# Performance work log

Measured on AMD Instinct MI355X. Metric: run time of the kernel, lower is better.

Reference implementation:

```python
import jax, jax.numpy as jnp
import numpy as np

LMAX = 6
NUM_COEFFS = (LMAX + 1) ** 2  # 49
REPEATS = np.array([2 * l + 1 for l in range(LMAX + 1)])  # coefficients per degree


def so3_linear(x, w, b):
    """Block-diagonal per-degree linear: x [N, 49, Cin], w [lmax+1, Cin, Cout], b [Cout].
    Bias is added only to the degree-0 (scalar) coefficient."""
    w_exp = jnp.repeat(w, REPEATS, axis=0)  # [49, Cin, Cout]
    out = jnp.einsum('nic,ico->nio', x, w_exp)
    return out.at[:, 0, :].add(b)


def setup_inputs() -> dict:
    key = jax.random.key(0)
    ks = jax.random.split(key, 10)
    N, C, H = 1024, 128, 256
    res = 18
    s = 0.05
    return {
        'node_feats': jax.random.normal(ks[0], (N, NUM_COEFFS, C), jnp.float32),
        'w1': jax.random.normal(ks[1], (LMAX + 1, C, H), jnp.float32) * s,
        'b1': jnp.zeros((H,), jnp.float32),
        'w2': jax.random.normal(ks[2], (LMAX + 1, H, C), jnp.float32) * s,
        'b2': jnp.zeros((C,), jnp.float32),
        'ws': jax.random.normal(ks[3], (C, H), jnp.float32) * s,
        'bs': jnp.zeros((H,), jnp.float32),
        'g1': jax.random.normal(ks[4], (H, H), jnp.float32) * s,
        'g2': jax.random.normal(ks[5], (H, H), jnp.float32) * s,
        'g3': jax.random.normal(ks[6], (H, H), jnp.float32) * s,
        'to_grid_mat': jax.random.normal(ks[7], (res, res, NUM_COEFFS), jnp.float32) * s,
        'from_grid_mat': jax.random.normal(ks[8], (res, res, NUM_COEFFS), jnp.float32) * s,
    }


def reference(node_feats, w1, b1, w2, b2, ws, bs, g1, g2, g3, to_grid_mat, from_grid_mat):
    # separable-S2 scalar gating branch: MLP on the l=0 coefficient  [N,1,H]
    gating = jax.nn.silu(jnp.einsum('nic,ch->nih', node_feats[:, 0:1], ws) + bs)
    # SO3 linear 1  [N,49,H]
    x = so3_linear(node_feats, w1, b1)
    # spherical harmonics -> grid  [N, beta, alpha, H]
    grid = jnp.einsum('bai,nih->nbah', to_grid_mat, x)
    # grid MLP (bias-free) with SiLU between layers
    grid = jax.nn.silu(jnp.einsum('nbah,hk->nbak', grid, g1))
    grid = jax.nn.silu(jnp.einsum('nbak,km->nbam', grid, g2))
    grid = jnp.einsum('nbam,mh->nbah', grid, g3)
    # grid -> spherical harmonics  [N,49,H]
    x = jnp.einsum('bai,nbah->nih', from_grid_mat, grid)
    # separable S2: replace l=0 component with gated scalars
    x = jnp.concatenate((gating, x[:, 1:]), axis=1)
    # SO3 linear 2  [N,49,C_out]
    return so3_linear(x, w2, b2)
```

## Files before the change

kernel.cpp:

```cpp
#include <hip/hip_runtime.h>
#include <hip/hip_bf16.h>

typedef __attribute__((ext_vector_type(8))) short bf16x8;
typedef __attribute__((ext_vector_type(4))) float f32x4;

#define MFMA(a,b,c) __builtin_amdgcn_mfma_f32_16x16x32_bf16((a),(b),(c),0,0,0)

#define WS_W1T 0
#define WS_W2T 229376
#define WS_G1T 458752
#define WS_TGP 655360
#define WS_FGT 679936
#define WS_TOTAL 704512

__device__ __forceinline__ ushort f2b(float f) {
  __hip_bfloat16 h = __float2bfloat16(f);
  ushort u; __builtin_memcpy(&u, &h, 2); return u;
}
__device__ __forceinline__ float silu_f(float x) { return x / (1.f + __expf(-x)); }
__device__ __forceinline__ bf16x8 ld8(const ushort* p) {
  return *reinterpret_cast<const bf16x8*>(p);
}

__global__ void prep_kernel(const float* __restrict__ w1, const float* __restrict__ w2,
                            const float* __restrict__ g1, const float* __restrict__ g2,
                            const float* __restrict__ g3, const float* __restrict__ tg,
                            const float* __restrict__ fg, ushort* __restrict__ o) {
  int idx = blockIdx.x * blockDim.x + threadIdx.x;
  if (idx >= WS_TOTAL) return;
  float v;
  if (idx < WS_W2T) {
    int l = idx >> 15, rem = idx & 32767, h = rem >> 7, c = rem & 127;
    v = w1[(l << 15) + c * 256 + h];
  } else if (idx < WS_G1T) {
    int j = idx - WS_W2T;
    int l = j >> 15, rem = j & 32767, oo = rem >> 8, h = rem & 255;
    v = w2[(l << 15) + h * 128 + oo];
  } else if (idx < WS_TGP) {
    int j = idx - WS_G1T;
    int m = j >> 16, r = j & 65535, n2 = r >> 8, k = r & 255;
    const float* g = (m == 0) ? g1 : ((m == 1) ? g2 : g3);
    v = g[k * 256 + n2];
  } else if (idx < WS_FGT) {
    int j = idx - WS_TGP, r = j >> 6, i2 = j & 63;
    v = (r < 324 && i2 < 49) ? tg[r * 49 + i2] : 0.f;
  } else {
    int j = idx - WS_FGT, i2 = j / 384, r = j % 384;
    v = (i2 < 49 && r < 324) ? fg[r * 49 + i2] : 0.f;
  }
  o[idx] = f2b(v);
}

__global__ __launch_bounds__(512, 1) void ffn_main(
    const float* __restrict__ nf, const float* __restrict__ b1,
    const float* __restrict__ b2, const float* __restrict__ wsg,
    const float* __restrict__ bs, const ushort* __restrict__ wbf,
    float* __restrict__ out)
{
  __shared__ __align__(16) ushort sm[35840];
  ushort* s_G   = sm;
  ushort* s_xbT = sm + 16896;
  float*  s_gat = reinterpret_cast<float*>(sm + 35328);
  ushort* s_GT  = s_xbT;
  ushort* s_nf  = s_G;
  ushort* s_xo  = s_G;

  const int tid  = threadIdx.x;
  const int lane = tid & 63;
  const int wv   = tid >> 6;
  const int lr   = lane & 15;
  const int lk   = lane >> 4;

  const float* nfp = nf + (size_t)blockIdx.x * 6272;

  {
    uint4 z = {0,0,0,0};
    for (int idx = tid; idx < 2304; idx += 512)
      *reinterpret_cast<uint4*>(&s_xbT[idx * 8]) = z;
    for (int idx = tid; idx < 52 * 32; idx += 512) {
      int r = idx >> 5, c4 = (idx & 31) << 2;
      float4 v = (r < 49) ? *reinterpret_cast<const float4*>(nfp + (r << 7) + c4)
                          : make_float4(0.f, 0.f, 0.f, 0.f);
      ushort4 pk = make_ushort4(f2b(v.x), f2b(v.y), f2b(v.z), f2b(v.w));
      *reinterpret_cast<ushort4*>(&s_nf[r * 136 + c4]) = pk;
    }
    if (tid < 256) {
      float a = bs[tid];
      #pragma unroll 4
      for (int c = 0; c < 128; ++c) a = fmaf(nfp[c], wsg[(c << 8) + tid], a);
      s_gat[tid] = silu_f(a);
    }
  }
  __syncthreads();

  {
    const ushort* w1T = wbf + WS_W1T;
    #pragma unroll 1
    for (int l = 0; l < 7; ++l) {
      f32x4 a0 = {0.f,0.f,0.f,0.f}, a1 = {0.f,0.f,0.f,0.f};
      const int arow = l * l + lr;
      const ushort* bb = w1T + (l << 15);
      #pragma unroll
      for (int ks = 0; ks < 4; ++ks) {
        bf16x8 af  = ld8(&s_nf[arow * 136 + ks * 32 + lk * 8]);
        bf16x8 bf0 = ld8(bb + ((wv * 32 + lr) << 7) + ks * 32 + lk * 8);
        bf16x8 bf1 = ld8(bb + ((wv * 32 + 16 + lr) << 7) + ks * 32 + lk * 8);
        a0 = MFMA(af, bf0, a0);
        a1 = MFMA(af, bf1, a1);
      }
      const int nv = 2 * l + 1;
      #pragma unroll
      for (int reg = 0; reg < 4; ++reg) {
        int il = lk * 4 + reg;
        if (il < nv) {
          int ig = l * l + il;
          int h0 = wv * 32 + lr, h1 = h0 + 16;
          s_xbT[h0 * 72 + ig] = f2b(a0[reg] + (ig == 0 ? b1[h0] : 0.f));
          s_xbT[h1 * 72 + ig] = f2b(a1[reg] + (ig == 0 ? b1[h1] : 0.f));
        }
      }
    }
  }
  __syncthreads();

  bf16x8 xbf[2][2];
  #pragma unroll
  for (int nt = 0; nt < 2; ++nt)
    #pragma unroll
    for (int ks = 0; ks < 2; ++ks)
      xbf[nt][ks] = ld8(&s_xbT[(wv * 32 + nt * 16 + lr) * 72 + ks * 32 + lk * 8]);

  f32x4 xo[4][2];
  #pragma unroll
  for (int mt = 0; mt < 4; ++mt)
    #pragma unroll
    for (int nt = 0; nt < 2; ++nt) xo[mt][nt] = (f32x4){0.f,0.f,0.f,0.f};

  const ushort* tgP = wbf + WS_TGP;
  const ushort* fgT = wbf + WS_FGT;

  #pragma unroll 1
  for (int ch = 0; ch < 6; ++ch) {
    {
      f32x4 c[4][2];
      #pragma unroll
      for (int mt = 0; mt < 4; ++mt)
        #pragma unroll
        for (int nt = 0; nt < 2; ++nt) c[mt][nt] = (f32x4){0.f,0.f,0.f,0.f};
      #pragma unroll
      for (int ks = 0; ks < 2; ++ks) {
        bf16x8 atg[4];
        #pragma unroll
        for (int mt = 0; mt < 4; ++mt)
          atg[mt] = ld8(tgP + ((ch * 64 + mt * 16 + lr) << 6) + ks * 32 + lk * 8);
        #pragma unroll
        for (int mt = 0; mt < 4; ++mt)
          #pragma unroll
          for (int nt = 0; nt < 2; ++nt) c[mt][nt] = MFMA(atg[mt], xbf[nt][ks], c[mt][nt]);
      }
      #pragma unroll
      for (int mt = 0; mt < 4; ++mt)
        #pragma unroll
        for (int nt = 0; nt < 2; ++nt)
          #pragma unroll
          for (int reg = 0; reg < 4; ++reg)
            s_G[(mt * 16 + lk * 4 + reg) * 264 + wv * 32 + nt * 16 + lr] = f2b(c[mt][nt][reg]);
    }
    __syncthreads();

    #pragma unroll 1
    for (int pass = 0; pass < 2; ++pass) {
      const ushort* gT = wbf + WS_G1T + (pass << 16);
      f32x4 c[4][2];
      #pragma unroll
      for (int mt = 0; mt < 4; ++mt)
        #pragma unroll
        for (int nt = 0; nt < 2; ++nt) c[mt][nt] = (f32x4){0.f,0.f,0.f,0.f};
      #pragma unroll
      for (int ks = 0; ks < 8; ++ks) {
        bf16x8 bstr[2];
        #pragma unroll
        for (int nt = 0; nt < 2; ++nt)
          bstr[nt] = ld8(gT + ((wv * 32 + nt * 16 + lr) << 8) + ks * 32 + lk * 8);
        bf16x8 af[4];
        #pragma unroll
        for (int mt = 0; mt < 4; ++mt)
          af[mt] = ld8(&s_G[(mt * 16 + lr) * 264 + ks * 32 + lk * 8]);
        #pragma unroll
        for (int mt = 0; mt < 4; ++mt)
          #pragma unroll
          for (int nt = 0; nt < 2; ++nt) c[mt][nt] = MFMA(af[mt], bstr[nt], c[mt][nt]);
      }
      __syncthreads();
      #pragma unroll
      for (int mt = 0; mt < 4; ++mt)
        #pragma unroll
        for (int nt = 0; nt < 2; ++nt)
          #pragma unroll
          for (int reg = 0; reg < 4; ++reg)
            s_G[(mt * 16 + lk * 4 + reg) * 264 + wv * 32 + nt * 16 + lr] = f2b(silu_f(c[mt][nt][reg]));
      __syncthreads();
    }

    {
      const ushort* g3T = wbf + WS_G1T + 131072;
      f32x4 c[4][2];
      #pragma unroll
      for (int mt = 0; mt < 4; ++mt)
        #pragma unroll
        for (int nt = 0; nt < 2; ++nt) c[mt][nt] = (f32x4){0.f,0.f,0.f,0.f};
      #pragma unroll
      for (int ks = 0; ks < 8; ++ks) {
        bf16x8 bstr[2];
        #pragma unroll
        for (int nt = 0; nt < 2; ++nt)
          bstr[nt] = ld8(g3T + ((wv * 32 + nt * 16 + lr) << 8) + ks * 32 + lk * 8);
        bf16x8 af[4];
        #pragma unroll
        for (int mt = 0; mt < 4; ++mt)
          af[mt] = ld8(&s_G[(mt * 16 + lr) * 264 + ks * 32 + lk * 8]);
        #pragma unroll
        for (int mt = 0; mt < 4; ++mt)
          #pragma unroll
          for (int nt = 0; nt < 2; ++nt) c[mt][nt] = MFMA(af[mt], bstr[nt], c[mt][nt]);
      }
      __syncthreads();
      #pragma unroll
      for (int mt = 0; mt < 4; ++mt)
        #pragma unroll
        for (int nt = 0; nt < 2; ++nt) {
          int h = wv * 32 + nt * 16 + lr;
          ushort4 pk = make_ushort4(f2b(c[mt][nt][0]), f2b(c[mt][nt][1]),
                                    f2b(c[mt][nt][2]), f2b(c[mt][nt][3]));
          *reinterpret_cast<ushort4*>(&s_GT[h * 72 + mt * 16 + lk * 4]) = pk;
        }
    }
    __syncthreads();

    {
      #pragma unroll
      for (int ks = 0; ks < 2; ++ks) {
        bf16x8 afg[4];
        #pragma unroll
        for (int mt = 0; mt < 4; ++mt)
          afg[mt] = ld8(fgT + (mt * 16 + lr) * 384 + ch * 64 + ks * 32 + lk * 8);
        bf16x8 bfr[2];
        #pragma unroll
        for (int nt = 0; nt < 2; ++nt)
          bfr[nt] = ld8(&s_GT[(wv * 32 + nt * 16 + lr) * 72 + ks * 32 + lk * 8]);
        #pragma unroll
        for (int mt = 0; mt < 4; ++mt)
          #pragma unroll
          for (int nt = 0; nt < 2; ++nt) xo[mt][nt] = MFMA(afg[mt], bfr[nt], xo[mt][nt]);
      }
    }
  }

  #pragma unroll
  for (int mt = 0; mt < 4; ++mt)
    #pragma unroll
    for (int nt = 0; nt < 2; ++nt)
      #pragma unroll
      for (int reg = 0; reg < 4; ++reg)
        s_xo[(mt * 16 + lk * 4 + reg) * 264 + wv * 32 + nt * 16 + lr] = f2b(xo[mt][nt][reg]);
  __syncthreads();
  if (tid < 256) s_xo[tid] = f2b(s_gat[tid]);
  __syncthreads();

  {
    const ushort* w2T = wbf + WS_W2T;
    float* outp = out + (size_t)blockIdx.x * 6272;
    #pragma unroll 1
    for (int l = 0; l < 7; ++l) {
      f32x4 acc = {0.f,0.f,0.f,0.f};
      const ushort* bb = w2T + (l << 15);
      const int arow = l * l + lr;
      #pragma unroll
      for (int ks = 0; ks < 8; ++ks) {
        bf16x8 af  = ld8(&s_xo[arow * 264 + ks * 32 + lk * 8]);
        bf16x8 bfr = ld8(bb + ((wv * 16 + lr) << 8) + ks * 32 + lk * 8);
        acc = MFMA(af, bfr, acc);
      }
      const int nv = 2 * l + 1;
      #pragma unroll
      for (int reg = 0; reg < 4; ++reg) {
        int il = lk * 4 + reg;
        if (il < nv) {
          int ig = l * l + il, o = wv * 16 + lr;
          outp[(ig << 7) + o] = acc[reg] + (ig == 0 ? b2[o] : 0.f);
        }
      }
    }
  }
}

extern "C" void kernel_launch(void* const* d_in, const int* in_sizes, int n_in,
                              void* d_out, int out_size, void* d_ws, size_t ws_size,
                              hipStream_t stream) {
  const float* nf  = (const float*)d_in[0];
  const float* w1  = (const float*)d_in[1];
  const float* b1  = (const float*)d_in[2];
  const float* w2  = (const float*)d_in[3];
  const float* b2  = (const float*)d_in[4];
  const float* wsg = (const float*)d_in[5];
  const float* bs  = (const float*)d_in[6];
  const float* g1  = (const float*)d_in[7];
  const float* g2  = (const float*)d_in[8];
  const float* g3  = (const float*)d_in[9];
  const float* tg  = (const float*)d_in[10];
  const float* fg  = (const float*)d_in[11];
  ushort* wbf = (ushort*)d_ws;
  float* out = (float*)d_out;

  prep_kernel<<<(WS_TOTAL + 255) / 256, 256, 0, stream>>>(w1, w2, g1, g2, g3, tg, fg, wbf);
  ffn_main<<<1024, 512, 0, stream>>>(nf, b1, b2, wsg, bs, wbf, out);
}
```

Before: 631.9 us.

## Double grid chunk size and swap MFMA operands for vectorized packed stores

Grid points are now processed in 3 chunks of 128 instead of 6 chunks of 64, so each weight fragment of g1/g2/g3 loaded from global memory is reused across twice as many rows and there are fewer barrier-separated stages. MFMA operands are swapped so accumulators come out transposed, which lets results go to LDS and the output as 4-wide packed ushort4/float4 stores instead of scalar stores. LDS use roughly doubles and register pressure rises with 8x2 accumulator tiles, which risks spills under the 512-thread launch bound.

```diff
diff --git a/kernel.cpp b/kernel.cpp
--- a/kernel.cpp
+++ b/kernel.cpp
@@ -20,6 +20,9 @@
 __device__ __forceinline__ float silu_f(float x) { return x / (1.f + __expf(-x)); }
 __device__ __forceinline__ bf16x8 ld8(const ushort* p) {
   return *reinterpret_cast<const bf16x8*>(p);
+}
+__device__ __forceinline__ ushort4 pk4(float a, float b, float c, float d) {
+  return make_ushort4(f2b(a), f2b(b), f2b(c), f2b(d));
 }
 
 __global__ void prep_kernel(const float* __restrict__ w1, const float* __restrict__ w2,
@@ -57,11 +60,11 @@
     const float* __restrict__ bs, const ushort* __restrict__ wbf,
     float* __restrict__ out)
 {
-  __shared__ __align__(16) ushort sm[35840];
+  __shared__ __align__(16) ushort sm[69120];
   ushort* s_G   = sm;
-  ushort* s_xbT = sm + 16896;
-  float*  s_gat = reinterpret_cast<float*>(sm + 35328);
-  ushort* s_GT  = s_xbT;
+  ushort* s_GT  = sm + 33792;
+  ushort* s_xbT = sm + 33792;
+  float*  s_gat = reinterpret_cast<float*>(sm + 68608);
   ushort* s_nf  = s_G;
   ushort* s_xo  = s_G;
 
@@ -81,8 +84,7 @@
       int r = idx >> 5, c4 = (idx & 31) << 2;
       float4 v = (r < 49) ? *reinterpret_cast<const float4*>(nfp + (r << 7) + c4)
                           : make_float4(0.f, 0.f, 0.f, 0.f);
-      ushort4 pk = make_ushort4(f2b(v.x), f2b(v.y), f2b(v.z), f2b(v.w));
-      *reinterpret_cast<ushort4*>(&s_nf[r * 136 + c4]) = pk;
+      *reinterpret_cast<ushort4*>(&s_nf[r * 136 + c4]) = pk4(v.x, v.y, v.z, v.w);
     }
     if (tid < 256) {
       float a = bs[tid];
@@ -140,40 +142,39 @@
   const ushort* fgT = wbf + WS_FGT;
 
   #pragma unroll 1
-  for (int ch = 0; ch < 6; ++ch) {
+  for (int ch = 0; ch < 3; ++ch) {
     {
-      f32x4 c[4][2];
-      #pragma unroll
-      for (int mt = 0; mt < 4; ++mt)
+      f32x4 c[8][2];
+      #pragma unroll
+      for (int mt = 0; mt < 8; ++mt)
         #pragma unroll
         for (int nt = 0; nt < 2; ++nt) c[mt][nt] = (f32x4){0.f,0.f,0.f,0.f};
       #pragma unroll
       for (int ks = 0; ks < 2; ++ks) {
-        bf16x8 atg[4];
-        #pragma unroll
-        for (int mt = 0; mt < 4; ++mt)
-          atg[mt] = ld8(tgP + ((ch * 64 + mt * 16 + lr) << 6) + ks * 32 + lk * 8);
-        #pragma unroll
-        for (int mt = 0; mt < 4; ++mt)
+        bf16x8 atg[8];
+        #pragma unroll
+        for (int mt = 0; mt < 8; ++mt)
+          atg[mt] = ld8(tgP + ((ch * 128 + mt * 16 + lr) << 6) + ks * 32 + lk * 8);
+        #pragma unroll
+        for (int mt = 0; mt < 8; ++mt)
           #pragma unroll
-          for (int nt = 0; nt < 2; ++nt) c[mt][nt] = MFMA(atg[mt], xbf[nt][ks], c[mt][nt]);
-      }
-      #pragma unroll
-      for (int mt = 0; mt < 4; ++mt)
-        #pragma unroll
-        for (int nt = 0; nt < 2; ++nt)
-          #pragma unroll
-          for (int reg = 0; reg < 4; ++reg)
-            s_G[(mt * 16 + lk * 4 + reg) * 264 + wv * 32 + nt * 16 + lr] = f2b(c[mt][nt][reg]);
+          for (int nt = 0; nt < 2; ++nt) c[mt][nt] = MFMA(xbf[nt][ks], atg[mt], c[mt][nt]);
+      }
+      #pragma unroll
+      for (int mt = 0; mt < 8; ++mt)
+        #pragma unroll
+        for (int nt = 0; nt < 2; ++nt)
+          *reinterpret_cast<ushort4*>(&s_G[(mt * 16 + lr) * 264 + wv * 32 + nt * 16 + lk * 4]) =
+              pk4(c[mt][nt][0], c[mt][nt][1], c[mt][nt][2], c[mt][nt][3]);
     }
     __syncthreads();
 
     #pragma unroll 1
     for (int pass = 0; pass < 2; ++pass) {
       const ushort* gT = wbf + WS_G1T + (pass << 16);
-      f32x4 c[4][2];
-      #pragma unroll
-      for (int mt = 0; mt < 4; ++mt)
+      f32x4 c[8][2];
+      #pragma unroll
+      for (int mt = 0; mt < 8; ++mt)
         #pragma unroll
         for (int nt = 0; nt < 2; ++nt) c[mt][nt] = (f32x4){0.f,0.f,0.f,0.f};
       #pragma unroll
@@ -182,76 +183,75 @@
         #pragma unroll
         for (int nt = 0; nt < 2; ++nt)
           bstr[nt] = ld8(gT + ((wv * 32 + nt * 16 + lr) << 8) + ks * 32 + lk * 8);
-        bf16x8 af[4];
+        bf16x8 af[8];
+        #pragma unroll
+        for (int mt = 0; mt < 8; ++mt)
+          af[mt] = ld8(&s_G[(mt * 16 + lr) * 264 + ks * 32 + lk * 8]);
+        #pragma unroll
+        for (int mt = 0; mt < 8; ++mt)
+          #pragma unroll
+          for (int nt = 0; nt < 2; ++nt) c[mt][nt] = MFMA(bstr[nt], af[mt], c[mt][nt]);
+      }
+      __syncthreads();
+      #pragma unroll
+      for (int mt = 0; mt < 8; ++mt)
+        #pragma unroll
+        for (int nt = 0; nt < 2; ++nt)
+          *reinterpret_cast<ushort4*>(&s_G[(mt * 16 + lr) * 264 + wv * 32 + nt * 16 + lk * 4]) =
+              pk4(silu_f(c[mt][nt][0]), silu_f(c[mt][nt][1]),
+                  silu_f(c[mt][nt][2]), silu_f(c[mt][nt][3]));
+      __syncthreads();
+    }
+
+    {
+      const ushort* g3T = wbf + WS_G1T + 131072;
+      f32x4 c[8][2];
+      #pragma unroll
+      for (int mt = 0; mt < 8; ++mt)
+        #pragma unroll
+        for (int nt = 0; nt < 2; ++nt) c[mt][nt] = (f32x4){0.f,0.f,0.f,0.f};
+      #pragma unroll
+      for (int ks = 0; ks < 8; ++ks) {
+        bf16x8 bstr[2];
+        #pragma unroll
+        for (int nt = 0; nt < 2; ++nt)
+          bstr[nt] = ld8(g3T + ((wv * 32 + nt * 16 + lr) << 8) + ks * 32 + lk * 8);
+        bf16x8 af[8];
+        #pragma unroll
+        for (int mt = 0; mt < 8; ++mt)
+          af[mt] = ld8(&s_G[(mt * 16 + lr) * 264 + ks * 32 + lk * 8]);
+        #pragma unroll
+        for (int mt = 0; mt < 8; ++mt)
+          #pragma unroll
+          for (int nt = 0; nt < 2; ++nt) c[mt][nt] = MFMA(af[mt], bstr[nt], c[mt][nt]);
+      }
+      __syncthreads();
+      #pragma unroll
+      for (int mt = 0; mt < 8; ++mt)
+        #pragma unroll
+        for (int nt = 0; nt < 2; ++nt) {
+          int h = wv * 32 + nt * 16 + lr;
+          *reinterpret_cast<ushort4*>(&s_GT[h * 136 + mt * 16 + lk * 4]) =
+              pk4(c[mt][nt][0], c[mt][nt][1], c[mt][nt][2], c[mt][nt][3]);
+        }
+    }
+    __syncthreads();
+
+    {
+      #pragma unroll
+      for (int ks = 0; ks < 4; ++ks) {
+        bf16x8 afg[4];
         #pragma unroll
         for (int mt = 0; mt < 4; ++mt)
-          af[mt] = ld8(&s_G[(mt * 16 + lr) * 264 + ks * 32 + lk * 8]);
+          afg[mt] = ld8(fgT + (mt * 16 + lr) * 384 + ch * 128 + ks * 32 + lk * 8);
+        bf16x8 bfr[2];
+        #pragma unroll
+        for (int nt = 0; nt < 2; ++nt)
+          bfr[nt] = ld8(&s_GT[(wv * 32 + nt * 16 + lr) * 136 + ks * 32 + lk * 8]);
         #pragma unroll
         for (int mt = 0; mt < 4; ++mt)
           #pragma unroll
-          for (int nt = 0; nt < 2; ++nt) c[mt][nt] = MFMA(af[mt], bstr[nt], c[mt][nt]);
-      }
-      __syncthreads();
-      #pragma unroll
-      for (int mt = 0; mt < 4; ++mt)
-        #pragma unroll
-        for (int nt = 0; nt < 2; ++nt)
-          #pragma unroll
-          for (int reg = 0; reg < 4; ++reg)
-            s_G[(mt * 16 + lk * 4 + reg) * 264 + wv * 32 + nt * 16 + lr] = f2b(silu_f(c[mt][nt][reg]));
-      __syncthreads();
-    }
-
-    {
-      const ushort* g3T = wbf + WS_G1T + 131072;
-      f32x4 c[4][2];
-      #pragma unroll
-      for (int mt = 0; mt < 4; ++mt)
-        #pragma unroll
-        for (int nt = 0; nt < 2; ++nt) c[mt][nt] = (f32x4){0.f,0.f,0.f,0.f};
-      #pragma unroll
-      for (int ks = 0; ks < 8; ++ks) {
-        bf16x8 bstr[2];
-        #pragma unroll
-        for (int nt = 0; nt < 2; ++nt)
-          bstr[nt] = ld8(g3T + ((wv * 32 + nt * 16 + lr) << 8) + ks * 32 + lk * 8);
-        bf16x8 af[4];
-        #pragma unroll
-        for (int mt = 0; mt < 4; ++mt)
-          af[mt] = ld8(&s_G[(mt * 16 + lr) * 264 + ks * 32 + lk * 8]);
-        #pragma unroll
-        for (int mt = 0; mt < 4; ++mt)
-          #pragma unroll
-          for (int nt = 0; nt < 2; ++nt) c[mt][nt] = MFMA(af[mt], bstr[nt], c[mt][nt]);
-      }
-      __syncthreads();
-      #pragma unroll
-      for (int mt = 0; mt < 4; ++mt)
-        #pragma unroll
-        for (int nt = 0; nt < 2; ++nt) {
-          int h = wv * 32 + nt * 16 + lr;
-          ushort4 pk = make_ushort4(f2b(c[mt][nt][0]), f2b(c[mt][nt][1]),
-                                    f2b(c[mt][nt][2]), f2b(c[mt][nt][3]));
-          *reinterpret_cast<ushort4*>(&s_GT[h * 72 + mt * 16 + lk * 4]) = pk;
-        }
-    }
-    __syncthreads();
-
-    {
-      #pragma unroll
-      for (int ks = 0; ks < 2; ++ks) {
-        bf16x8 afg[4];
-        #pragma unroll
-        for (int mt = 0; mt < 4; ++mt)
-          afg[mt] = ld8(fgT + (mt * 16 + lr) * 384 + ch * 64 + ks * 32 + lk * 8);
-        bf16x8 bfr[2];
-        #pragma unroll
-        for (int nt = 0; nt < 2; ++nt)
-          bfr[nt] = ld8(&s_GT[(wv * 32 + nt * 16 + lr) * 72 + ks * 32 + lk * 8]);
-        #pragma unroll
-        for (int mt = 0; mt < 4; ++mt)
-          #pragma unroll
-          for (int nt = 0; nt < 2; ++nt) xo[mt][nt] = MFMA(afg[mt], bfr[nt], xo[mt][nt]);
+          for (int nt = 0; nt < 2; ++nt) xo[mt][nt] = MFMA(bfr[nt], afg[mt], xo[mt][nt]);
       }
     }
   }
@@ -260,9 +260,8 @@
   for (int mt = 0; mt < 4; ++mt)
     #pragma unroll
     for (int nt = 0; nt < 2; ++nt)
-      #pragma unroll
-      for (int reg = 0; reg < 4; ++reg)
-        s_xo[(mt * 16 + lk * 4 + reg) * 264 + wv * 32 + nt * 16 + lr] = f2b(xo[mt][nt][reg]);
+      *reinterpret_cast<ushort4*>(&s_xo[(mt * 16 + lr) * 264 + wv * 32 + nt * 16 + lk * 4]) =
+          pk4(xo[mt][nt][0], xo[mt][nt][1], xo[mt][nt][2], xo[mt][nt][3]);
   __syncthreads();
   if (tid < 256) s_xo[tid] = f2b(s_gat[tid]);
   __syncthreads();
@@ -270,6 +269,7 @@
   {
     const ushort* w2T = wbf + WS_W2T;
     float* outp = out + (size_t)blockIdx.x * 6272;
+    const float4 bb2 = *reinterpret_cast<const float4*>(b2 + wv * 16 + lk * 4);
     #pragma unroll 1
     for (int l = 0; l < 7; ++l) {
       f32x4 acc = {0.f,0.f,0.f,0.f};
@@ -277,18 +277,15 @@
       const int arow = l * l + lr;
       #pragma unroll
       for (int ks = 0; ks < 8; ++ks) {
-        bf16x8 af  = ld8(&s_xo[arow * 264 + ks * 32 + lk * 8]);
-        bf16x8 bfr = ld8(bb + ((wv * 16 + lr) << 8) + ks * 32 + lk * 8);
-        acc = MFMA(af, bfr, acc);
-      }
-      const int nv = 2 * l + 1;
-      #pragma unroll
-      for (int reg = 0; reg < 4; ++reg) {
-        int il = lk * 4 + reg;
-        if (il < nv) {
-          int ig = l * l + il, o = wv * 16 + lr;
-          outp[(ig << 7) + o] = acc[reg] + (ig == 0 ? b2[o] : 0.f);
-        }
+        bf16x8 xf = ld8(&s_xo[arow * 264 + ks * 32 + lk * 8]);
+        bf16x8 wf = ld8(bb + ((wv * 16 + lr) << 8) + ks * 32 + lk * 8);
+        acc = MFMA(wf, xf, acc);
+      }
+      if (lr < 2 * l + 1) {
+        int ig = l * l + lr;
+        float4 v = make_float4(acc[0], acc[1], acc[2], acc[3]);
+        if (ig == 0) { v.x += bb2.x; v.y += bb2.y; v.z += bb2.z; v.w += bb2.w; }
+        *reinterpret_cast<float4*>(outp + (ig << 7) + wv * 16 + lk * 4) = v;
       }
     }
   }
```

Result: faster. 555.9 us (-12.0%).
